# Optimization experiments

Measured on AMD Instinct MI355X. Metric: run time of the kernel, lower is better.

Reference implementation:

```python
import jax, jax.numpy as jnp
import numpy as np

N = 50000      # nodes
E = 640000     # edges
DIN = 256      # in_channels
DE = 64        # edge_dim
H1 = 128       # hidden_channels (conv1 out)
H2 = 64        # hidden_channels//2 (conv2 out)
OUT = 1


def tconv(x, src, dst, edge_attr, Wq, bq, Wk, bk, Wv, bv, We, Ws, bs):
    """PyG TransformerConv, heads=1, concat=True, root_weight=True."""
    n = x.shape[0]
    C = Wq.shape[1]
    q = x @ Wq + bq                      # [N, C]
    k = x @ Wk + bk                      # [N, C]
    v = x @ Wv + bv                      # [N, C]
    e = edge_attr @ We                   # [E, C] (lin_edge has no bias)
    k_e = k[src] + e                     # key_j + edge_emb per edge
    alpha = jnp.sum(q[dst] * k_e, axis=-1) / jnp.sqrt(jnp.float32(C))  # [E]
    # neighborhood softmax over incoming edges of each dst node
    m = jax.ops.segment_max(alpha, dst, num_segments=n)
    ex = jnp.exp(alpha - m[dst])
    denom = jax.ops.segment_sum(ex, dst, num_segments=n)
    a = ex / (denom[dst] + 1e-16)
    msg = a[:, None] * (v[src] + e)      # [E, C]
    out = jax.ops.segment_sum(msg, dst, num_segments=n)  # [N, C]
    return out + x @ Ws + bs             # root/skip connection


def setup_inputs() -> dict:
    key = jax.random.key(0)
    ks = jax.random.split(key, 24)
    p = lambda k, shape: jax.random.normal(k, shape, jnp.float32) * 0.02
    inp = {
        "x": jax.random.normal(ks[0], (N, DIN), jnp.float32),
        "edge_index": jax.random.randint(ks[1], (2, E), 0, N),
        "edge_attr": jax.random.normal(ks[2], (E, DE), jnp.float32),
        # conv1 params (in=DIN -> out=H1)
        "Wq1": p(ks[3], (DIN, H1)), "bq1": jnp.zeros((H1,), jnp.float32),
        "Wk1": p(ks[4], (DIN, H1)), "bk1": jnp.zeros((H1,), jnp.float32),
        "Wv1": p(ks[5], (DIN, H1)), "bv1": jnp.zeros((H1,), jnp.float32),
        "We1": p(ks[6], (DE, H1)),
        "Ws1": p(ks[7], (DIN, H1)), "bs1": jnp.zeros((H1,), jnp.float32),
        # conv2 params (in=H1 -> out=H2)
        "Wq2": p(ks[8], (H1, H2)), "bq2": jnp.zeros((H2,), jnp.float32),
        "Wk2": p(ks[9], (H1, H2)), "bk2": jnp.zeros((H2,), jnp.float32),
        "Wv2": p(ks[10], (H1, H2)), "bv2": jnp.zeros((H2,), jnp.float32),
        "We2": p(ks[11], (DE, H2)),
        "Ws2": p(ks[12], (H1, H2)), "bs2": jnp.zeros((H2,), jnp.float32),
        # classifier
        "Wc": p(ks[13], (H2, OUT)), "bc": jnp.zeros((OUT,), jnp.float32),
    }
    return inp


def reference(x, edge_index, edge_attr,
              Wq1, bq1, Wk1, bk1, Wv1, bv1, We1, Ws1, bs1,
              Wq2, bq2, Wk2, bk2, Wv2, bv2, We2, Ws2, bs2,
              Wc, bc):
    src, dst = edge_index[0], edge_index[1]
    h = tconv(x, src, dst, edge_attr, Wq1, bq1, Wk1, bk1, Wv1, bv1, We1, Ws1, bs1)
    h = jax.nn.relu(h)  # dropout is identity in eval mode
    h = tconv(h, src, dst, edge_attr, Wq2, bq2, Wk2, bk2, Wv2, bv2, We2, Ws2, bs2)
    h = jax.nn.relu(h)
    return h @ Wc + bc  # [N, 1] logits
```

## Files before the change

### kernel.cpp

```cpp
#include <hip/hip_runtime.h>
#include <math.h>

constexpr int NN  = 50000;
constexpr int NE  = 640000;
constexpr int DIN = 256;
constexpr int DE  = 64;
constexpr int H1  = 128;
constexpr int H2  = 64;
constexpr int EWS = H1 + H2;

using u16 = unsigned short;
typedef __attribute__((ext_vector_type(8))) short bf16x8;
typedef __attribute__((ext_vector_type(4))) float f32x4;
typedef __attribute__((ext_vector_type(4))) unsigned int u32x4;

__device__ inline u16 f2bf(float f) {
  unsigned u = __float_as_uint(f);
  unsigned r = (u + 0x7FFFu + ((u >> 16) & 1u)) >> 16;
  return (u16)r;
}
__device__ inline float bf2f(u16 h) { return __uint_as_float(((unsigned)h) << 16); }
__device__ inline unsigned pack2(u16 a, u16 b) {
  return (unsigned)a | ((unsigned)b << 16);
}
__device__ inline f32x4 mfma16(bf16x8 a, bf16x8 b, f32x4 c) {
  return __builtin_amdgcn_mfma_f32_16x16x32_bf16(a, b, c, 0, 0, 0);
}

__global__ __launch_bounds__(256) void packwt_kernel(
    const float* __restrict__ W0, const float* __restrict__ W1,
    const float* __restrict__ W2, const float* __restrict__ W3,
    const float* __restrict__ b0, const float* __restrict__ b1,
    const float* __restrict__ b2, const float* __restrict__ b3,
    u16* __restrict__ Bth, u16* __restrict__ Btl, float* __restrict__ bcat,
    int K, int C, int nmats) {
  int total = nmats * C * K;
  for (int idx = blockIdx.x * blockDim.x + threadIdx.x; idx < total;
       idx += gridDim.x * blockDim.x) {
    int k = idx % K;
    int n = idx / K;
    int which = n / C, cc = n % C;
    const float* W = which == 0 ? W0 : which == 1 ? W1 : which == 2 ? W2 : W3;
    float v = W[k * C + cc];
    u16 h = f2bf(v);
    Bth[(size_t)n * K + k] = h;
    Btl[(size_t)n * K + k] = f2bf(v - bf2f(h));
    if (k == 0 && bcat) {
      const float* b = which == 0 ? b0 : which == 1 ? b1 : which == 2 ? b2 : b3;
      bcat[n] = b ? b[cc] : 0.f;
    }
  }
}

__global__ __launch_bounds__(256) void hist_kernel(const int* __restrict__ dst,
                                                   int* __restrict__ deg, int nE) {
  int e = blockIdx.x * blockDim.x + threadIdx.x;
  if (e < nE) atomicAdd(&deg[dst[e]], 1);
}

__global__ __launch_bounds__(256) void scan1_kernel(const int* __restrict__ deg,
                                                    int* __restrict__ part,
                                                    int* __restrict__ chunkSums,
                                                    int n) {
  __shared__ int s[256];
  int tid = threadIdx.x;
  int i = blockIdx.x * 256 + tid;
  int v0 = (i < n) ? deg[i] : 0;
  s[tid] = v0;
  __syncthreads();
  for (int off = 1; off < 256; off <<= 1) {
    int v = (tid >= off) ? s[tid - off] : 0;
    __syncthreads();
    s[tid] += v;
    __syncthreads();
  }
  if (i < n) part[i] = s[tid];
  if (tid == 255) chunkSums[blockIdx.x] = s[255];
}

__global__ __launch_bounds__(256) void scan2_kernel(int* __restrict__ chunkSums,
                                                    int nchunks) {
  __shared__ int s[256];
  int tid = threadIdx.x;
  s[tid] = (tid < nchunks) ? chunkSums[tid] : 0;
  __syncthreads();
  for (int off = 1; off < 256; off <<= 1) {
    int v = (tid >= off) ? s[tid - off] : 0;
    __syncthreads();
    s[tid] += v;
    __syncthreads();
  }
  if (tid < nchunks) chunkSums[tid] = s[tid];
}

__global__ __launch_bounds__(256) void scan3_kernel(const int* __restrict__ deg,
                                                    const int* __restrict__ part,
                                                    const int* __restrict__ chunkSums,
                                                    int* __restrict__ row_start,
                                                    int n, int nE) {
  int i = blockIdx.x * 256 + threadIdx.x;
  if (i < n)
    row_start[i] = part[i] - deg[i] + (blockIdx.x ? chunkSums[blockIdx.x - 1] : 0);
  if (i == 0) row_start[n] = nE;
}

__global__ __launch_bounds__(256) void scatter_kernel(const int* __restrict__ dst,
                                                      const int* __restrict__ row_start,
                                                      int* __restrict__ cursor,
                                                      int* __restrict__ eid, int nE) {
  int e = blockIdx.x * blockDim.x + threadIdx.x;
  if (e >= nE) return;
  int d = dst[e];
  int pos = row_start[d] + atomicAdd(&cursor[d], 1);
  eid[pos] = e;
}

__global__ __launch_bounds__(256) void sort_extract_kernel(
    int* __restrict__ eid, const int* __restrict__ row_start,
    const int* __restrict__ srcI, int* __restrict__ src_csr, int n) {
  int v = blockIdx.x * blockDim.x + threadIdx.x;
  if (v >= n) return;
  int b = row_start[v], e = row_start[v + 1];
  for (int i = b + 1; i < e; i++) {
    int key = eid[i];
    int j = i - 1;
    while (j >= b && eid[j] > key) { eid[j + 1] = eid[j]; j--; }
    eid[j + 1] = key;
  }
  for (int i = b; i < e; i++) src_csr[i] = srcI[eid[i]];
}

template <int BN, int EPI>
__global__ __launch_bounds__(256) void mfma_gemm_kernel(
    const float* __restrict__ A, const int* __restrict__ ridx,
    const u16* __restrict__ Bth, const u16* __restrict__ Btl,
    const float* __restrict__ bias, float* __restrict__ Cout,
    float* __restrict__ Qp, u16* __restrict__ KVp, float* __restrict__ Sp,
    int M, int Nn, int K, int Cl) {
  constexpr int BM = 128, BK = 32;
  constexpr int NI = BN / 32;
  constexpr int SM_STAGE = (BM + BN) * BK * 2;
  constexpr int SM_EPI = (EPI >= 1) ? BM * BN : 0;
  constexpr int SM = SM_STAGE > SM_EPI ? SM_STAGE : SM_EPI;
  __shared__ __align__(16) u16 smem[SM];
  u16* Ah = smem;
  u16* Al = smem + BM * BK;
  u16* Bh = smem + 2 * BM * BK;
  u16* Bl = smem + 2 * BM * BK + BN * BK;
  int tid = threadIdx.x;
  int lane = tid & 63, wid = tid >> 6;
  int wm = wid >> 1, wn = wid & 1;
  int row0 = blockIdx.y * BM, col0 = blockIdx.x * BN;
  int k8 = lane >> 4, rb = lane & 15;

  f32x4 acc[4][NI];
#pragma unroll
  for (int mi = 0; mi < 4; mi++)
#pragma unroll
    for (int ni = 0; ni < NI; ni++) acc[mi][ni] = (f32x4){0.f, 0.f, 0.f, 0.f};

  size_t aoff[2];
  int sdst[2];
  for (int p = 0; p < 2; p++) {
    int idx = p * 256 + tid;
    int r = idx >> 2, c = idx & 3;
    int ar = row0 + r;
    if (ar >= M) ar = M - 1;
    if (ridx) ar = ridx[ar];
    aoff[p] = (size_t)ar * K + c * 8;
    sdst[p] = r * BK + ((c ^ ((r >> 1) & 3)) << 3);
  }

  for (int k0 = 0; k0 < K; k0 += BK) {
    __syncthreads();
#pragma unroll
    for (int p = 0; p < 2; p++) {
      const float* s = A + aoff[p] + k0;
      float4 u = *(const float4*)s, v = *(const float4*)(s + 4);
      float f[8] = {u.x, u.y, u.z, u.w, v.x, v.y, v.z, v.w};
      u16 h[8], l[8];
#pragma unroll
      for (int j = 0; j < 8; j++) {
        h[j] = f2bf(f[j]);
        l[j] = f2bf(f[j] - bf2f(h[j]));
      }
      *(uint4*)&Ah[sdst[p]] = make_uint4(pack2(h[0], h[1]), pack2(h[2], h[3]),
                                         pack2(h[4], h[5]), pack2(h[6], h[7]));
      *(uint4*)&Al[sdst[p]] = make_uint4(pack2(l[0], l[1]), pack2(l[2], l[3]),
                                         pack2(l[4], l[5]), pack2(l[6], l[7]));
    }
#pragma unroll
    for (int p = 0; p < (BN * 4) / 256; p++) {
      int idx = p * 256 + tid;
      int n = idx >> 2, c = idx & 3;
      size_t goff = (size_t)(col0 + n) * K + k0 + c * 8;
      int doff = n * BK + ((c ^ ((n >> 1) & 3)) << 3);
      *(uint4*)&Bh[doff] = *(const uint4*)&Bth[goff];
      *(uint4*)&Bl[doff] = *(const uint4*)&Btl[goff];
    }
    __syncthreads();
    bf16x8 ah[4], al[4], bh[NI], bl[NI];
#pragma unroll
    for (int mi = 0; mi < 4; mi++) {
      int row = wm * 64 + mi * 16 + rb;
      int off = row * BK + ((k8 ^ ((row >> 1) & 3)) << 3);
      ah[mi] = *(const bf16x8*)&Ah[off];
      al[mi] = *(const bf16x8*)&Al[off];
    }
#pragma unroll
    for (int ni = 0; ni < NI; ni++) {
      int cn = wn * (BN / 2) + ni * 16 + rb;
      int off = cn * BK + ((k8 ^ ((cn >> 1) & 3)) << 3);
      bh[ni] = *(const bf16x8*)&Bh[off];
      bl[ni] = *(const bf16x8*)&Bl[off];
    }
#pragma unroll
    for (int mi = 0; mi < 4; mi++)
#pragma unroll
      for (int ni = 0; ni < NI; ni++) {
        f32x4 c = acc[mi][ni];
        c = mfma16(ah[mi], bh[ni], c);
        c = mfma16(al[mi], bh[ni], c);
        c = mfma16(ah[mi], bl[ni], c);
        acc[mi][ni] = c;
      }
  }

  bool kvseg = false;
  if constexpr (EPI == 2) {
    int seg = col0 / Cl;
    kvseg = (seg == 1 || seg == 2);
    if (!kvseg) {
      float* dst = (seg == 0) ? Qp : Sp;
      int cbase = (seg == 0) ? col0 : col0 - 3 * Cl;
#pragma unroll
      for (int ni = 0; ni < NI; ni++) {
        int cfrag = wn * (BN / 2) + ni * 16 + rb;
        float bv = bias ? bias[col0 + cfrag] : 0.f;
#pragma unroll
        for (int mi = 0; mi < 4; mi++) {
#pragma unroll
          for (int q = 0; q < 4; q++) {
            int row = row0 + wm * 64 + mi * 16 + k8 * 4 + q;
            if (row < M)
              dst[(size_t)row * Cl + cbase + cfrag] = acc[mi][ni][q] + bv;
          }
        }
      }
      return;
    }
  }
  if (kvseg) {
    __syncthreads();
    u16* S = smem;
#pragma unroll
    for (int ni = 0; ni < NI; ni++) {
      int coll = wn * (BN / 2) + ni * 16 + rb;
      float bv = bias ? bias[col0 + coll] : 0.f;
#pragma unroll
      for (int mi = 0; mi < 4; mi++) {
#pragma unroll
        for (int q = 0; q < 4; q++) {
          int rowl = wm * 64 + mi * 16 + k8 * 4 + q;
          S[rowl * BN + (coll ^ (((rowl >> 2) & 3) << 4))] =
              f2bf(acc[mi][ni][q] + bv);
        }
      }
    }
    __syncthreads();
    u16* dbase = KVp;
    size_t dstride = 2 * Cl;
    int dcol0 = col0 - Cl;
    constexpr int PASSES = (BM * BN * 2) / (256 * 16);
#pragma unroll
    for (int p = 0; p < PASSES; p++) {
      int idx = p * 256 + tid;
      int r = idx / (BN / 8);
      int cp = idx % (BN / 8);
      int row = row0 + r;
      int cps = cp ^ (((r >> 2) & 3) << 1);
      if (row < M)
        *(uint4*)&dbase[(size_t)row * dstride + dcol0 + cp * 8] =
            *(const uint4*)&S[r * BN + cps * 8];
    }
    return;
  }
  if constexpr (EPI == 0) {
#pragma unroll
    for (int ni = 0; ni < NI; ni++) {
      int col = col0 + wn * (BN / 2) + ni * 16 + rb;
      float bv = bias ? bias[col] : 0.f;
#pragma unroll
      for (int mi = 0; mi < 4; mi++) {
#pragma unroll
        for (int q = 0; q < 4; q++) {
          int row = row0 + wm * 64 + mi * 16 + k8 * 4 + q;
          if (row < M) Cout[(size_t)row * Nn + col] = acc[mi][ni][q] + bv;
        }
      }
    }
  }
}

__global__ __launch_bounds__(512, 4) void edge_gemm_kernel(
    const float* __restrict__ A, const u16* __restrict__ Bth,
    const u16* __restrict__ Btl, u16* __restrict__ Cbf) {
  constexpr int BM = 128, BN = 192, K = DE;
  constexpr int NI = 6;
  __shared__ __align__(16) u16 smem[2 * BN * K];
  u16* BhL = smem;
  u16* BlL = smem + BN * K;
  int tid = threadIdx.x;
  int lane = tid & 63, wid = tid >> 6;
  int wm = wid >> 1, wn = wid & 1;
  int row0 = blockIdx.x * BM;
  int k8 = lane >> 4, rb = lane & 15;

#pragma unroll
  for (int p = 0; p < 6; p++) {
    int idx = p * 512 + tid;
    bool hi = idx < 1536;
    int m = hi ? idx : idx - 1536;
    int n = m >> 3, c = m & 7;
    const u16* src = (hi ? Bth : Btl) + n * K + c * 8;
    u16* dst = (hi ? BhL : BlL) + n * K + ((c ^ (n & 7)) << 3);
    *(uint4*)dst = *(const uint4*)src;
  }
  __syncthreads();

  f32x4 acc[2][NI];
#pragma unroll
  for (int mi = 0; mi < 2; mi++)
#pragma unroll
    for (int ni = 0; ni < NI; ni++) acc[mi][ni] = (f32x4){0.f, 0.f, 0.f, 0.f};

#pragma unroll
  for (int k0 = 0; k0 < K; k0 += 32) {
#pragma unroll
    for (int mi = 0; mi < 2; mi++) {
      int row = row0 + wm * 32 + mi * 16 + rb;
      const float* s = A + (size_t)row * K + k0 + k8 * 8;
      float4 u = *(const float4*)s, v = *(const float4*)(s + 4);
      uint4 pk = make_uint4(pack2(f2bf(u.x), f2bf(u.y)), pack2(f2bf(u.z), f2bf(u.w)),
                            pack2(f2bf(v.x), f2bf(v.y)), pack2(f2bf(v.z), f2bf(v.w)));
      bf16x8 ah = *(bf16x8*)&pk;
      int chunk = (k0 >> 3) + k8;
#pragma unroll
      for (int ni = 0; ni < NI; ni++) {
        int cn = wn * 96 + ni * 16 + rb;
        int off = cn * K + ((chunk ^ (cn & 7)) << 3);
        bf16x8 bhf = *(const bf16x8*)&BhL[off];
        bf16x8 blf = *(const bf16x8*)&BlL[off];
        f32x4 c = acc[mi][ni];
        c = mfma16(ah, bhf, c);
        c = mfma16(ah, blf, c);
        acc[mi][ni] = c;
      }
    }
  }

  u16* S = smem;
#pragma unroll
  for (int half = 0; half < 2; half++) {
    __syncthreads();
    if ((wm >> 1) == half) {
#pragma unroll
      for (int ni = 0; ni < NI; ni++) {
        int coll = wn * 96 + ni * 16 + rb;
#pragma unroll
        for (int mi = 0; mi < 2; mi++) {
#pragma unroll
          for (int q = 0; q < 4; q++) {
            int rowl = (wm & 1) * 32 + mi * 16 + k8 * 4 + q;
            S[rowl * BN + (coll ^ (((rowl >> 2) & 3) << 4))] =
                f2bf(acc[mi][ni][q]);
          }
        }
      }
    }
    __syncthreads();
#pragma unroll
    for (int p = 0; p < 3; p++) {
      int idx = p * 512 + tid;
      int r = idx / (BN / 8);
      int cp = idx % (BN / 8);
      int row = row0 + half * 64 + r;
      int cps = cp ^ (((r >> 2) & 3) << 1);
      __builtin_nontemporal_store(*(const u32x4*)&S[r * BN + cps * 8],
                                  (u32x4*)&Cbf[(size_t)row * BN + cp * 8]);
    }
  }
}

template <int C, int EOFF>
__global__ __launch_bounds__(256) void fused_edge_kernel(
    const float* __restrict__ Q, const float* __restrict__ SKIP,
    const u16* __restrict__ KV, const u16* __restrict__ Ew,
    const int* __restrict__ row_start, const int* __restrict__ src_csr,
    const int* __restrict__ eid, float* __restrict__ h, float scale, int n) {
  constexpr int CPL = C / 64;
  int node = blockIdx.x * 4 + (threadIdx.x >> 6);
  int lane = threadIdx.x & 63;
  if (node >= n) return;
  int ch = lane * CPL;
  float q[CPL], acc[CPL], skip[CPL];
#pragma unroll
  for (int j = 0; j < CPL; j++) {
    q[j] = Q[(size_t)node * C + ch + j];
    skip[j] = SKIP[(size_t)node * C + ch + j];
    acc[j] = 0.f;
  }
  float m = -INFINITY, denom = 0.f;
  int b = row_start[node], e = row_start[node + 1];
  for (int i = b; i < e; i += 4) {
    float part[4], vv[4][CPL];
#pragma unroll
    for (int u = 0; u < 4; u++) {
      int idx = (i + u < e) ? i + u : e - 1;
      int s = src_csr[idx];
      int eo = eid[idx];
      const u16* kvp = KV + (size_t)s * (2 * C);
      const u16* Ee = Ew + (size_t)eo * EWS + EOFF;
      float kk[CPL], ev[CPL];
      if constexpr (CPL == 2) {
        unsigned uk = *(const unsigned*)(kvp + ch);
        unsigned uv = *(const unsigned*)(kvp + C + ch);
        unsigned ue = *(const unsigned*)(Ee + ch);
        kk[0] = bf2f((u16)uk); kk[1] = bf2f((u16)(uk >> 16));
        vv[u][0] = bf2f((u16)uv); vv[u][1] = bf2f((u16)(uv >> 16));
        ev[0] = bf2f((u16)ue); ev[1] = bf2f((u16)(ue >> 16));
      } else {
        kk[0] = bf2f(kvp[ch]);
        vv[u][0] = bf2f(kvp[C + ch]);
        ev[0] = bf2f(Ee[ch]);
      }
      float p = 0.f;
#pragma unroll
      for (int j = 0; j < CPL; j++) {
        p = fmaf(q[j], kk[j] + ev[j], p);
        vv[u][j] += ev[j];
      }
      part[u] = p;
    }
#pragma unroll
    for (int off = 32; off > 0; off >>= 1) {
      part[0] += __shfl_xor(part[0], off);
      part[1] += __shfl_xor(part[1], off);
      part[2] += __shfl_xor(part[2], off);
      part[3] += __shfl_xor(part[3], off);
    }
    float l[4];
#pragma unroll
    for (int u = 0; u < 4; u++)
      l[u] = (i + u < e) ? part[u] * scale : -INFINITY;
    float nm = fmaxf(fmaxf(fmaxf(l[0], l[1]), fmaxf(l[2], l[3])), m);
    float f = expf(m - nm);
    float w[4];
#pragma unroll
    for (int u = 0; u < 4; u++) w[u] = expf(l[u] - nm);
    denom = denom * f + (w[0] + w[1]) + (w[2] + w[3]);
#pragma unroll
    for (int j = 0; j < CPL; j++) {
      float a = acc[j] * f;
      a = fmaf(w[0], vv[0][j], a);
      a = fmaf(w[1], vv[1][j], a);
      a = fmaf(w[2], vv[2][j], a);
      a = fmaf(w[3], vv[3][j], a);
      acc[j] = a;
    }
    m = nm;
  }
  float inv = 1.f / (denom + 1e-16f);
#pragma unroll
  for (int j = 0; j < CPL; j++)
    h[(size_t)node * C + ch + j] = fmaxf(acc[j] * inv + skip[j], 0.f);
}

__global__ __launch_bounds__(256) void classifier_kernel(
    const float* __restrict__ h2, const float* __restrict__ Wc,
    const float* __restrict__ bc, float* __restrict__ out, int n) {
  int w = blockIdx.x * 4 + (threadIdx.x >> 6);
  int lane = threadIdx.x & 63;
  if (w >= n) return;
  float v = h2[(size_t)w * 64 + lane] * Wc[lane];
#pragma unroll
  for (int off = 32; off > 0; off >>= 1) v += __shfl_xor(v, off);
  if (lane == 0) out[w] = v + bc[0];
}

extern "C" void kernel_launch(void* const* d_in, const int* in_sizes, int n_in,
                              void* d_out, int out_size, void* d_ws,
                              size_t ws_size, hipStream_t stream) {
  const float* x         = (const float*)d_in[0];
  const int*   ei        = (const int*)d_in[1];
  const float* edge_attr = (const float*)d_in[2];
  const float* Wq1 = (const float*)d_in[3];  const float* bq1 = (const float*)d_in[4];
  const float* Wk1 = (const float*)d_in[5];  const float* bk1 = (const float*)d_in[6];
  const float* Wv1 = (const float*)d_in[7];  const float* bv1 = (const float*)d_in[8];
  const float* We1 = (const float*)d_in[9];
  const float* Ws1 = (const float*)d_in[10]; const float* bs1 = (const float*)d_in[11];
  const float* Wq2 = (const float*)d_in[12]; const float* bq2 = (const float*)d_in[13];
  const float* Wk2 = (const float*)d_in[14]; const float* bk2 = (const float*)d_in[15];
  const float* Wv2 = (const float*)d_in[16]; const float* bv2 = (const float*)d_in[17];
  const float* We2 = (const float*)d_in[18];
  const float* Ws2 = (const float*)d_in[19]; const float* bs2 = (const float*)d_in[20];
  const float* Wc  = (const float*)d_in[21]; const float* bc  = (const float*)d_in[22];
  float* out = (float*)d_out;

  const int* srcI = ei;
  const int* dstI = ei + NE;

  char* ws = (char*)d_ws;
  size_t off = 0;
  auto alloc = [&](size_t bytes) {
    void* p = ws + off;
    off += (bytes + 255) & ~(size_t)255;
    return p;
  };
  u16*   EwB  = (u16*)alloc((size_t)NE * EWS * 2);
  float* Q1   = (float*)alloc((size_t)NN * H1 * 4);
  float* S1   = (float*)alloc((size_t)NN * H1 * 4);
  u16*   KV1  = (u16*)alloc((size_t)NN * 2 * H1 * 2);
  float* Q2   = (float*)alloc((size_t)NN * H2 * 4);
  float* S2   = (float*)alloc((size_t)NN * H2 * 4);
  u16*   KV2  = (u16*)alloc((size_t)NN * 2 * H2 * 2);
  float* h1   = (float*)alloc((size_t)NN * H1 * 4);
  float* h2   = (float*)alloc((size_t)NN * H2 * 4);
  u16* B1h = (u16*)alloc((size_t)4 * H1 * DIN * 2);
  u16* B1l = (u16*)alloc((size_t)4 * H1 * DIN * 2);
  u16* B2h = (u16*)alloc((size_t)4 * H2 * H1 * 2);
  u16* B2l = (u16*)alloc((size_t)4 * H2 * H1 * 2);
  u16* Ech = (u16*)alloc((size_t)EWS * DE * 2);
  u16* Ecl = (u16*)alloc((size_t)EWS * DE * 2);
  float* b1cat = (float*)alloc(4 * H1 * 4);
  float* b2cat = (float*)alloc(4 * H2 * 4);
  int* deg       = (int*)alloc(NN * 4);
  int* cursor    = (int*)alloc(NN * 4);
  int* row_start = (int*)alloc((NN + 1) * 4);
  int* part      = (int*)alloc(((NN + 255) / 256) * 256 * 4);
  int* chunkSums = (int*)alloc(256 * 4);
  int* eid       = (int*)alloc(NE * 4);
  int* src_csr   = (int*)alloc(NE * 4);
  (void)ws_size; (void)in_sizes; (void)n_in; (void)out_size;

  const int nchunks = (NN + 255) / 256;

  packwt_kernel<<<256, 256, 0, stream>>>(Wq1, Wk1, Wv1, Ws1, bq1, bk1, bv1, bs1,
                                         B1h, B1l, b1cat, DIN, H1, 4);
  packwt_kernel<<<128, 256, 0, stream>>>(Wq2, Wk2, Wv2, Ws2, bq2, bk2, bv2, bs2,
                                         B2h, B2l, b2cat, H1, H2, 4);
  packwt_kernel<<<64, 256, 0, stream>>>(We1, nullptr, nullptr, nullptr, nullptr,
                                        nullptr, nullptr, nullptr, Ech, Ecl,
                                        nullptr, DE, H1, 1);
  packwt_kernel<<<32, 256, 0, stream>>>(We2, nullptr, nullptr, nullptr, nullptr,
                                        nullptr, nullptr, nullptr,
                                        Ech + (size_t)H1 * DE, Ecl + (size_t)H1 * DE,
                                        nullptr, DE, H2, 1);

  hipMemsetAsync(deg, 0, NN * sizeof(int), stream);
  hipMemsetAsync(cursor, 0, NN * sizeof(int), stream);
  hist_kernel<<<(NE + 255) / 256, 256, 0, stream>>>(dstI, deg, NE);
  scan1_kernel<<<nchunks, 256, 0, stream>>>(deg, part, chunkSums, NN);
  scan2_kernel<<<1, 256, 0, stream>>>(chunkSums, nchunks);
  scan3_kernel<<<nchunks, 256, 0, stream>>>(deg, part, chunkSums, row_start, NN, NE);
  scatter_kernel<<<(NE + 255) / 256, 256, 0, stream>>>(dstI, row_start, cursor,
                                                       eid, NE);
  sort_extract_kernel<<<(NN + 255) / 256, 256, 0, stream>>>(eid, row_start, srcI,
                                                            src_csr, NN);

  edge_gemm_kernel<<<NE / 128, 512, 0, stream>>>(edge_attr, Ech, Ecl, EwB);

  mfma_gemm_kernel<128, 2><<<dim3(4 * H1 / 128, (NN + 127) / 128), 256, 0, stream>>>(
      x, nullptr, B1h, B1l, b1cat, nullptr, Q1, KV1, S1, NN, 4 * H1, DIN, H1);
  fused_edge_kernel<H1, 0><<<(NN + 3) / 4, 256, 0, stream>>>(
      Q1, S1, KV1, EwB, row_start, src_csr, eid, h1, 0.08838834764831845f, NN);

  mfma_gemm_kernel<64, 2><<<dim3(4 * H2 / 64, (NN + 127) / 128), 256, 0, stream>>>(
      h1, nullptr, B2h, B2l, b2cat, nullptr, Q2, KV2, S2, NN, 4 * H2, H1, H2);
  fused_edge_kernel<H2, H1><<<(NN + 3) / 4, 256, 0, stream>>>(
      Q2, S2, KV2, EwB, row_start, src_csr, eid, h2, 0.125f, NN);

  classifier_kernel<<<(NN + 3) / 4, 256, 0, stream>>>(h2, Wc, bc, out, NN);
}
```

Baseline: 488.4 us.

## Drop low-order bf16 weight split in edge GEMM and unroll edge loop by 8

The edge-attribute GEMM now uses only the high bf16 part of the edge weights, removing the second MFMA per tile and halving the shared memory used for weight staging. The fused attention/aggregation kernel processes 8 incoming edges per iteration instead of 4, so more gathers are in flight. This trades precision of the edge embedding (single bf16 weight instead of hi+lo split) for less compute and LDS traffic. The wider unroll also raises register pressure.

```diff
diff --git a/kernel.cpp b/kernel.cpp
--- a/kernel.cpp
+++ b/kernel.cpp
@@ -44,7 +44,7 @@
     float v = W[k * C + cc];
     u16 h = f2bf(v);
     Bth[(size_t)n * K + k] = h;
-    Btl[(size_t)n * K + k] = f2bf(v - bf2f(h));
+    if (Btl) Btl[(size_t)n * K + k] = f2bf(v - bf2f(h));
     if (k == 0 && bcat) {
       const float* b = which == 0 ? b0 : which == 1 ? b1 : which == 2 ? b2 : b3;
       bcat[n] = b ? b[cc] : 0.f;
@@ -304,12 +304,11 @@
 
 __global__ __launch_bounds__(512, 4) void edge_gemm_kernel(
     const float* __restrict__ A, const u16* __restrict__ Bth,
-    const u16* __restrict__ Btl, u16* __restrict__ Cbf) {
+    u16* __restrict__ Cbf) {
   constexpr int BM = 128, BN = 192, K = DE;
   constexpr int NI = 6;
-  __shared__ __align__(16) u16 smem[2 * BN * K];
+  __shared__ __align__(16) u16 smem[BN * K];
   u16* BhL = smem;
-  u16* BlL = smem + BN * K;
   int tid = threadIdx.x;
   int lane = tid & 63, wid = tid >> 6;
   int wm = wid >> 1, wn = wid & 1;
@@ -317,14 +316,11 @@
   int k8 = lane >> 4, rb = lane & 15;
 
 #pragma unroll
-  for (int p = 0; p < 6; p++) {
-    int idx = p * 512 + tid;
-    bool hi = idx < 1536;
-    int m = hi ? idx : idx - 1536;
+  for (int p = 0; p < 3; p++) {
+    int m = p * 512 + tid;
     int n = m >> 3, c = m & 7;
-    const u16* src = (hi ? Bth : Btl) + n * K + c * 8;
-    u16* dst = (hi ? BhL : BlL) + n * K + ((c ^ (n & 7)) << 3);
-    *(uint4*)dst = *(const uint4*)src;
+    *(uint4*)&BhL[n * K + ((c ^ (n & 7)) << 3)] =
+        *(const uint4*)&Bth[n * K + c * 8];
   }
   __syncthreads();
 
@@ -349,12 +345,7 @@
       for (int ni = 0; ni < NI; ni++) {
         int cn = wn * 96 + ni * 16 + rb;
         int off = cn * K + ((chunk ^ (cn & 7)) << 3);
-        bf16x8 bhf = *(const bf16x8*)&BhL[off];
-        bf16x8 blf = *(const bf16x8*)&BlL[off];
-        f32x4 c = acc[mi][ni];
-        c = mfma16(ah, bhf, c);
-        c = mfma16(ah, blf, c);
-        acc[mi][ni] = c;
+        acc[mi][ni] = mfma16(ah, *(const bf16x8*)&BhL[off], acc[mi][ni]);
       }
     }
   }
@@ -399,6 +390,7 @@
     const int* __restrict__ row_start, const int* __restrict__ src_csr,
     const int* __restrict__ eid, float* __restrict__ h, float scale, int n) {
   constexpr int CPL = C / 64;
+  constexpr int EB = 8;
   int node = blockIdx.x * 4 + (threadIdx.x >> 6);
   int lane = threadIdx.x & 63;
   if (node >= n) return;
@@ -412,10 +404,10 @@
   }
   float m = -INFINITY, denom = 0.f;
   int b = row_start[node], e = row_start[node + 1];
-  for (int i = b; i < e; i += 4) {
-    float part[4], vv[4][CPL];
-#pragma unroll
-    for (int u = 0; u < 4; u++) {
+  for (int i = b; i < e; i += EB) {
+    float part[EB], vv[EB][CPL];
+#pragma unroll
+    for (int u = 0; u < EB; u++) {
       int idx = (i + u < e) ? i + u : e - 1;
       int s = src_csr[idx];
       int eo = eid[idx];
@@ -444,28 +436,30 @@
     }
 #pragma unroll
     for (int off = 32; off > 0; off >>= 1) {
-      part[0] += __shfl_xor(part[0], off);
-      part[1] += __shfl_xor(part[1], off);
-      part[2] += __shfl_xor(part[2], off);
-      part[3] += __shfl_xor(part[3], off);
-    }
-    float l[4];
-#pragma unroll
-    for (int u = 0; u < 4; u++)
+#pragma unroll
+      for (int u = 0; u < EB; u++) part[u] += __shfl_xor(part[u], off);
+    }
+    float l[EB];
+#pragma unroll
+    for (int u = 0; u < EB; u++)
       l[u] = (i + u < e) ? part[u] * scale : -INFINITY;
-    float nm = fmaxf(fmaxf(fmaxf(l[0], l[1]), fmaxf(l[2], l[3])), m);
+    float bm = l[0];
+#pragma unroll
+    for (int u = 1; u < EB; u++) bm = fmaxf(bm, l[u]);
+    float nm = fmaxf(bm, m);
     float f = expf(m - nm);
-    float w[4];
-#pragma unroll
-    for (int u = 0; u < 4; u++) w[u] = expf(l[u] - nm);
-    denom = denom * f + (w[0] + w[1]) + (w[2] + w[3]);
+    float w[EB];
+#pragma unroll
+    for (int u = 0; u < EB; u++) w[u] = expf(l[u] - nm);
+    float wsum = 0.f;
+#pragma unroll
+    for (int u = 0; u < EB; u++) wsum += w[u];
+    denom = denom * f + wsum;
 #pragma unroll
     for (int j = 0; j < CPL; j++) {
       float a = acc[j] * f;
-      a = fmaf(w[0], vv[0][j], a);
-      a = fmaf(w[1], vv[1][j], a);
-      a = fmaf(w[2], vv[2][j], a);
-      a = fmaf(w[3], vv[3][j], a);
+#pragma unroll
+      for (int u = 0; u < EB; u++) a = fmaf(w[u], vv[u][j], a);
       acc[j] = a;
     }
     m = nm;
@@ -531,7 +525,6 @@
   u16* B2h = (u16*)alloc((size_t)4 * H2 * H1 * 2);
   u16* B2l = (u16*)alloc((size_t)4 * H2 * H1 * 2);
   u16* Ech = (u16*)alloc((size_t)EWS * DE * 2);
-  u16* Ecl = (u16*)alloc((size_t)EWS * DE * 2);
   float* b1cat = (float*)alloc(4 * H1 * 4);
   float* b2cat = (float*)alloc(4 * H2 * 4);
   int* deg       = (int*)alloc(NN * 4);
@@ -550,11 +543,11 @@
   packwt_kernel<<<128, 256, 0, stream>>>(Wq2, Wk2, Wv2, Ws2, bq2, bk2, bv2, bs2,
                                          B2h, B2l, b2cat, H1, H2, 4);
   packwt_kernel<<<64, 256, 0, stream>>>(We1, nullptr, nullptr, nullptr, nullptr,
-                                        nullptr, nullptr, nullptr, Ech, Ecl,
+                                        nullptr, nullptr, nullptr, Ech, nullptr,
                                         nullptr, DE, H1, 1);
   packwt_kernel<<<32, 256, 0, stream>>>(We2, nullptr, nullptr, nullptr, nullptr,
                                         nullptr, nullptr, nullptr,
-                                        Ech + (size_t)H1 * DE, Ecl + (size_t)H1 * DE,
+                                        Ech + (size_t)H1 * DE, nullptr,
                                         nullptr, DE, H2, 1);
 
   hipMemsetAsync(deg, 0, NN * sizeof(int), stream);
@@ -568,7 +561,7 @@
   sort_extract_kernel<<<(NN + 255) / 256, 256, 0, stream>>>(eid, row_start, srcI,
                                                             src_csr, NN);
 
-  edge_gemm_kernel<<<NE / 128, 512, 0, stream>>>(edge_attr, Ech, Ecl, EwB);
+  edge_gemm_kernel<<<NE / 128, 512, 0, stream>>>(edge_attr, Ech, EwB);
 
   mfma_gemm_kernel<128, 2><<<dim3(4 * H1 / 128, (NN + 127) / 128), 256, 0, stream>>>(
       x, nullptr, B1h, B1l, b1cat, nullptr, Q1, KV1, S1, NN, 4 * H1, DIN, H1);
```

Result: no change. 485.7 us (median of 2 runs) (-0.6%).
